# Optimization experiments

Measured on AMD Instinct MI355X. Metric: run time of the kernel, lower is better.

The kernel has to match this reference:

```python
import jax, jax.numpy as jnp
import numpy as np

D_MODEL = 1024
N_HEADS = 16
D_K = D_MODEL // N_HEADS
B, S = 2, 2048


def setup_inputs() -> dict:
    key = jax.random.key(0)
    ks = jax.random.split(key, 11)
    def lin(kw, kb, fan_in):
        bound = 1.0 / np.sqrt(fan_in)
        W = jax.random.uniform(kw, (fan_in, D_MODEL), jnp.float32, -bound, bound)
        b = jax.random.uniform(kb, (D_MODEL,), jnp.float32, -bound, bound)
        return W, b
    Wq, bq = lin(ks[0], ks[1], D_MODEL)
    Wk, bk = lin(ks[2], ks[3], D_MODEL)
    Wv, bv = lin(ks[4], ks[5], D_MODEL)
    Wo, bo = lin(ks[6], ks[7], D_MODEL)
    q = jax.random.normal(ks[8], (B, S, D_MODEL), jnp.float32)
    k = jax.random.normal(ks[9], (B, S, D_MODEL), jnp.float32)
    v = jax.random.normal(ks[10], (B, S, D_MODEL), jnp.float32)
    return {"q": q, "k": k, "v": v,
            "Wq": Wq, "bq": bq, "Wk": Wk, "bk": bk,
            "Wv": Wv, "bv": bv, "Wo": Wo, "bo": bo}


def reference(q, k, v, Wq, bq, Wk, bk, Wv, bv, Wo, bo):
    Bz, Sq, _ = q.shape
    def split_heads(x):  # [B,S,D] -> [B,H,S,d_k]
        return x.reshape(x.shape[0], x.shape[1], N_HEADS, D_K).transpose(0, 2, 1, 3)
    qh = split_heads(q @ Wq + bq)
    kh = split_heads(k @ Wk + bk)
    vh = split_heads(v @ Wv + bv)
    scores = jnp.einsum("bhqd,bhkd->bhqk", qh, kh) / jnp.sqrt(jnp.float32(D_K))
    attn = jax.nn.softmax(scores, axis=-1)
    out = jnp.einsum("bhqk,bhkd->bhqd", attn, vh)
    out = out.transpose(0, 2, 1, 3).reshape(Bz, Sq, D_MODEL)
    return out @ Wo + bo
```

## Files before the change

kernel.cpp:

```cpp
#include <hip/hip_runtime.h>
#include <hip/hip_bf16.h>
#include <stdint.h>

typedef __bf16 bf16;
typedef __bf16 bf16x8 __attribute__((ext_vector_type(8)));
typedef __bf16 bf16x4 __attribute__((ext_vector_type(4)));
typedef float  f32x4  __attribute__((ext_vector_type(4)));
typedef float  f32x16 __attribute__((ext_vector_type(16)));
typedef uint32_t u32;

#define MFMA16(a,b,c) __builtin_amdgcn_mfma_f32_16x16x32_bf16((a),(b),(c),0,0,0)
#define MFMA32(a,b,c) __builtin_amdgcn_mfma_f32_32x32x16_bf16((a),(b),(c),0,0,0)

#define QSCL 0.1803368801111204f

__device__ __forceinline__ u32 sx32(u32 x) {
    return (u32)__shfl_xor((int)x, 32, 64);
}
__device__ __forceinline__ float swapred_max(float v) {
    return fmaxf(v, __builtin_bit_cast(float, sx32(__builtin_bit_cast(u32, v))));
}
__device__ __forceinline__ float swapred_sum(float v) {
    return v + __builtin_bit_cast(float, sx32(__builtin_bit_cast(u32, v)));
}
__device__ __forceinline__ u32 pkbf(float lo, float hi) {
    union { bf16 h[2]; u32 u; } un;
    un.h[0] = (bf16)lo; un.h[1] = (bf16)hi;
    return un.u;
}
__device__ __forceinline__ void pack_frags(const float* p, int hi, bf16x8& f0, bf16x8& f1) {
    u32 k01 = pkbf(p[0],  p[1]),  k23 = pkbf(p[2],  p[3]);
    u32 k45 = pkbf(p[4],  p[5]),  k67 = pkbf(p[6],  p[7]);
    u32 k89 = pkbf(p[8],  p[9]),  kab = pkbf(p[10], p[11]);
    u32 kcd = pkbf(p[12], p[13]), kef = pkbf(p[14], p[15]);
    u32 x01 = sx32(k01), x23 = sx32(k23), x45 = sx32(k45), x67 = sx32(k67);
    u32 x89 = sx32(k89), xab = sx32(kab), xcd = sx32(kcd), xef = sx32(kef);
    union { u32 w[4]; bf16x8 v; } u0, u1;
    u0.w[0] = hi ? x45 : k01;  u0.w[1] = hi ? x67 : k23;
    u0.w[2] = hi ? k45 : x01;  u0.w[3] = hi ? k67 : x23;
    u1.w[0] = hi ? xcd : k89;  u1.w[1] = hi ? xef : kab;
    u1.w[2] = hi ? kcd : x89;  u1.w[3] = hi ? kef : xab;
    f0 = u0.v; f1 = u1.v;
}

__global__ __launch_bounds__(256) void k_cvt3(const float* __restrict__ a, const float* __restrict__ b,
                                              const float* __restrict__ c,
                                              bf16* __restrict__ x, bf16* __restrict__ y,
                                              bf16* __restrict__ z) {
    int i = blockIdx.x * 256 + threadIdx.x;
    int t = i >> 20;
    int r = (i & 1048575) << 2;
    const float* s = (t == 0) ? a : ((t == 1) ? b : c);
    bf16* d = (t == 0) ? x : ((t == 1) ? y : z);
    float4 v = *(const float4*)&s[r];
    bf16x4 w = {(bf16)v.x, (bf16)v.y, (bf16)v.z, (bf16)v.w};
    *(bf16x4*)&d[r] = w;
}
__global__ __launch_bounds__(256) void k_cvt1(const float* __restrict__ s, bf16* __restrict__ d) {
    int r = (blockIdx.x * 256 + threadIdx.x) << 2;
    float4 v = *(const float4*)&s[r];
    bf16x4 w = {(bf16)v.x, (bf16)v.y, (bf16)v.z, (bf16)v.w};
    *(bf16x4*)&d[r] = w;
}

__global__ __launch_bounds__(256) void k_transpose_w(const float* __restrict__ W,
                                                     bf16* __restrict__ Wt, float scale) {
    __shared__ bf16 t[64][65];
    const int n0 = blockIdx.x * 64, k0 = blockIdx.y * 64;
    for (int i = 0; i < 16; ++i) {
        int idx = threadIdx.x + i * 256, r = idx >> 6, c = idx & 63;
        t[r][c] = (bf16)(W[(size_t)(k0 + r) * 1024 + n0 + c] * scale);
    }
    __syncthreads();
    for (int i = 0; i < 16; ++i) {
        int idx = threadIdx.x + i * 256, r = idx >> 6, c = idx & 63;
        Wt[(size_t)(n0 + r) * 1024 + k0 + c] = t[c][r];
    }
}

__global__ __launch_bounds__(256) void k_transpose_v(const bf16* __restrict__ V,
                                                     bf16* __restrict__ Vt) {
    __shared__ bf16 t[64][65];
    const int s0 = blockIdx.x * 64, bh = blockIdx.y;
    for (int i = 0; i < 16; ++i) {
        int idx = threadIdx.x + i * 256, r = idx >> 6, c = idx & 63;
        t[r][c] = V[((size_t)bh * 2048 + s0 + r) * 64 + c];
    }
    __syncthreads();
    for (int i = 0; i < 16; ++i) {
        int idx = threadIdx.x + i * 256, r = idx >> 6, c = idx & 63;
        Vt[((size_t)bh * 64 + r) * 2048 + s0 + c] = t[c][r];
    }
}

__device__ __forceinline__ void gemm_tile(const bf16* __restrict__ A, const bf16* __restrict__ Bt,
                                          const float* __restrict__ bias, float bscale,
                                          void* __restrict__ Cp, int out_mode, int m0, int n0,
                                          bf16 (*As)[64], bf16 (*Bs)[64]) {
    const int tid = threadIdx.x;
    const int wid = tid >> 6, lane = tid & 63, lg = lane >> 4, lm = lane & 15;
    const int wr = wid >> 1, wc = wid & 1;
    const int grow = tid >> 3, gcol = (tid & 7) << 3;

    f32x4 acc[4][4] = {};

    for (int kt = 0; kt < 16; ++kt) {
        const int k0 = kt << 6;
        __syncthreads();
#pragma unroll
        for (int p = 0; p < 4; ++p) {
            __builtin_amdgcn_global_load_lds(
                (const __attribute__((address_space(1))) void*)(A + (size_t)(m0 + p * 32 + grow) * 1024 + k0 + gcol),
                (__attribute__((address_space(3))) void*)(&As[p * 32 + wid * 8][0]), 16, 0, 0);
            __builtin_amdgcn_global_load_lds(
                (const __attribute__((address_space(1))) void*)(Bt + (size_t)(n0 + p * 32 + grow) * 1024 + k0 + gcol),
                (__attribute__((address_space(3))) void*)(&Bs[p * 32 + wid * 8][0]), 16, 0, 0);
        }
        __syncthreads();
#pragma unroll
        for (int kk = 0; kk < 2; ++kk) {
            bf16x8 a[4], b[4];
#pragma unroll
            for (int i = 0; i < 4; ++i) a[i] = *(const bf16x8*)&As[wr * 64 + i * 16 + lm][kk * 32 + lg * 8];
#pragma unroll
            for (int j = 0; j < 4; ++j) b[j] = *(const bf16x8*)&Bs[wc * 64 + j * 16 + lm][kk * 32 + lg * 8];
#pragma unroll
            for (int i = 0; i < 4; ++i)
#pragma unroll
                for (int j = 0; j < 4; ++j) acc[i][j] = MFMA16(a[i], b[j], acc[i][j]);
        }
    }

    for (int i = 0; i < 4; ++i) {
        for (int j = 0; j < 4; ++j) {
            int col = n0 + wc * 64 + j * 16 + lm;
            float bv = bscale * bias[col];
            for (int q = 0; q < 4; ++q) {
                int row = m0 + wr * 64 + i * 16 + lg * 4 + q;
                float val = acc[i][j][q] + bv;
                if (out_mode == 0) {
                    int bb = row >> 11, s = row & 2047, h = col >> 6, d = col & 63;
                    ((bf16*)Cp)[(((size_t)bb * 16 + h) * 2048 + s) * 64 + d] = (bf16)val;
                } else {
                    ((float*)Cp)[(size_t)row * 1024 + col] = (float)val;
                }
            }
        }
    }
}

__device__ __forceinline__ void tile_decode(int r, int& m0, int& n0) {
    int xcd = r & 7, slot = (r >> 3) & 3, n = (r >> 5) & 7;
    m0 = (xcd * 4 + slot) * 128;
    n0 = n * 128;
}

__global__ __launch_bounds__(256, 4) void k_gemm_one(const bf16* __restrict__ A,
                                                     const bf16* __restrict__ Bt,
                                                     const float* __restrict__ bias, float bscale,
                                                     void* __restrict__ Cp, int out_mode) {
    __shared__ bf16 As[128][64];
    __shared__ bf16 Bs[128][64];
    int m0, n0;
    tile_decode(blockIdx.x, m0, n0);
    gemm_tile(A, Bt, bias, bscale, Cp, out_mode, m0, n0, As, Bs);
}

__global__ __launch_bounds__(256, 4) void k_gemm_qkv(const bf16* __restrict__ qc, const bf16* __restrict__ kc,
                                                     const bf16* __restrict__ vc,
                                                     const bf16* __restrict__ Wtq, const bf16* __restrict__ Wtk,
                                                     const bf16* __restrict__ Wtv,
                                                     const float* __restrict__ bq, const float* __restrict__ bk,
                                                     const float* __restrict__ bv,
                                                     bf16* __restrict__ Qb, bf16* __restrict__ Kb,
                                                     bf16* __restrict__ Vb) {
    __shared__ bf16 As[128][64];
    __shared__ bf16 Bs[128][64];
    int l = blockIdx.x, z = l >> 8, r = l & 255;
    int m0, n0;
    tile_decode(r, m0, n0);
    const bf16* A  = (z == 0) ? qc : ((z == 1) ? kc : vc);
    const bf16* Bt = (z == 0) ? Wtq : ((z == 1) ? Wtk : Wtv);
    const float* bias = (z == 0) ? bq : ((z == 1) ? bk : bv);
    float bscale = (z == 0) ? QSCL : 1.0f;
    bf16* Cp = (z == 0) ? Qb : ((z == 1) ? Kb : Vb);
    gemm_tile(A, Bt, bias, bscale, (void*)Cp, 0, m0, n0, As, Bs);
}

__global__ __launch_bounds__(512, 2) void k_attn(const bf16* __restrict__ Q,
                                                 const bf16* __restrict__ Kb,
                                                 const bf16* __restrict__ Vt,
                                                 bf16* __restrict__ Out) {
    __shared__ bf16 Ks[2][64 * 64];
    __shared__ bf16 Vs[2][64 * 64];
    const int tid = threadIdx.x;
    const int wid = tid >> 6, lane = tid & 63;
    const int lm = lane & 31, hi = lane >> 5;
    const int bid = blockIdx.x;
    const int bh = bid & 31, qt = bid >> 5;
    const int bb = bh >> 4, h = bh & 15;
    const int qrow = qt * 256 + wid * 32 + lm;
    const size_t qk_base = (size_t)bh * (2048 * 64);
    const size_t vt_base = (size_t)bh * (64 * 2048);

    const int srow = tid >> 3, sc8 = tid & 7;
    const int cse = (sc8 ^ (srow & 7)) * 8;
    const bf16* kstage = Kb + qk_base + (size_t)srow * 64 + cse;
    const bf16* vstage = Vt + vt_base + (size_t)srow * 2048 + cse;
    const int ldsoff = wid * 1024;

    bf16x8 qf[4];
    {
        const bf16* qp = Q + qk_base + (size_t)qrow * 64 + hi * 8;
#pragma unroll
        for (int f = 0; f < 4; ++f) qf[f] = *(const bf16x8*)(qp + f * 16);
    }

    f32x16 O0 = {}, O1 = {};
    float mrow = -1e30f, lrow = 0.f;

    const int swz = (lm & 7);

    __builtin_amdgcn_global_load_lds(
        (const __attribute__((address_space(1))) void*)(kstage),
        (__attribute__((address_space(3))) void*)((char*)&Ks[0][0] + ldsoff), 16, 0, 0);
    __builtin_amdgcn_global_load_lds(
        (const __attribute__((address_space(1))) void*)(vstage),
        (__attribute__((address_space(3))) void*)((char*)&Vs[0][0] + ldsoff), 16, 0, 0);
    __syncthreads();

    int cur = 0;
#pragma unroll 1
    for (int kt = 0; kt < 32; ++kt) {
        if (kt + 1 < 32) {
            __builtin_amdgcn_global_load_lds(
                (const __attribute__((address_space(1))) void*)(kstage + (size_t)(kt + 1) * 4096),
                (__attribute__((address_space(3))) void*)((char*)&Ks[cur ^ 1][0] + ldsoff), 16, 0, 0);
            __builtin_amdgcn_global_load_lds(
                (const __attribute__((address_space(1))) void*)(vstage + (size_t)(kt + 1) * 64),
                (__attribute__((address_space(3))) void*)((char*)&Vs[cur ^ 1][0] + ldsoff), 16, 0, 0);
        }

        const char* Ksc = (const char*)&Ks[cur][0];
        const char* Vsc = (const char*)&Vs[cur][0];

        bf16x8 kf0[4], kf1[4];
#pragma unroll
        for (int f = 0; f < 4; ++f) {
            int ch = (f << 1) | hi;
            kf0[f] = *(const bf16x8*)(Ksc + lm * 128 + ((ch ^ swz) << 4));
            kf1[f] = *(const bf16x8*)(Ksc + (lm + 32) * 128 + ((ch ^ swz) << 4));
        }
        bf16x8 vf0[4], vf1[4];
#pragma unroll
        for (int ks = 0; ks < 4; ++ks) {
            int ch = (ks << 1) | hi;
            vf0[ks] = *(const bf16x8*)(Vsc + lm * 128 + ((ch ^ swz) << 4));
            vf1[ks] = *(const bf16x8*)(Vsc + (lm + 32) * 128 + ((ch ^ swz) << 4));
        }

        f32x16 s0 = {}, s1 = {};
#pragma unroll
        for (int f = 0; f < 4; ++f) {
            s0 = MFMA32(kf0[f], qf[f], s0);
            s1 = MFMA32(kf1[f], qf[f], s1);
        }

        float t8[8];
#pragma unroll
        for (int r = 0; r < 8; ++r)
            t8[r] = fmaxf(fmaxf(s0[r], s0[r + 8]), fmaxf(s1[r], s1[r + 8]));
#pragma unroll
        for (int st = 4; st; st >>= 1)
#pragma unroll
            for (int r = 0; r < st; ++r) t8[r] = fmaxf(t8[r], t8[r + st]);
        float pm = swapred_max(t8[0]);

        if (!__all(pm <= mrow + 8.0f)) {
            float mnew = fmaxf(mrow, pm);
            float corr = __builtin_amdgcn_exp2f(mrow - mnew);
            lrow *= corr;
            O0 *= corr;
            O1 *= corr;
            mrow = mnew;
        }

        float p0a[16], p1a[16];
#pragma unroll
        for (int r = 0; r < 16; ++r) p0a[r] = __builtin_amdgcn_exp2f(s0[r] - mrow);
#pragma unroll
        for (int r = 0; r < 16; ++r) p1a[r] = __builtin_amdgcn_exp2f(s1[r] - mrow);
        float u8[8];
#pragma unroll
        for (int r = 0; r < 8; ++r) u8[r] = (p0a[r] + p0a[r + 8]) + (p1a[r] + p1a[r + 8]);
#pragma unroll
        for (int st = 4; st; st >>= 1)
#pragma unroll
            for (int r = 0; r < st; ++r) u8[r] = u8[r] + u8[r + st];
        lrow += swapred_sum(u8[0]);

        bf16x8 pf[4];
        pack_frags(p0a, hi, pf[0], pf[1]);
        pack_frags(p1a, hi, pf[2], pf[3]);

#pragma unroll
        for (int ks = 0; ks < 4; ++ks) {
            O0 = MFMA32(vf0[ks], pf[ks], O0);
            O1 = MFMA32(vf1[ks], pf[ks], O1);
        }

        __syncthreads();
        cur ^= 1;
    }

    float inv = 1.0f / lrow;
    bf16* op = Out + ((size_t)bb * 2048 + qrow) * 1024 + h * 64 + 4 * hi;
#pragma unroll
    for (int t = 0; t < 4; ++t) {
        bf16x4 w0, w1;
#pragma unroll
        for (int e = 0; e < 4; ++e) {
            w0[e] = (bf16)(O0[4 * t + e] * inv);
            w1[e] = (bf16)(O1[4 * t + e] * inv);
        }
        *(bf16x4*)(op + 8 * t)      = w0;
        *(bf16x4*)(op + 32 + 8 * t) = w1;
    }
}

extern "C" void kernel_launch(void* const* d_in, const int* in_sizes, int n_in,
                              void* d_out, int out_size, void* d_ws, size_t ws_size,
                              hipStream_t stream) {
    const float* q  = (const float*)d_in[0];
    const float* k  = (const float*)d_in[1];
    const float* v  = (const float*)d_in[2];
    const float* Wq = (const float*)d_in[3];
    const float* bq = (const float*)d_in[4];
    const float* Wk = (const float*)d_in[5];
    const float* bk = (const float*)d_in[6];
    const float* Wv = (const float*)d_in[7];
    const float* bv = (const float*)d_in[8];
    const float* Wo = (const float*)d_in[9];
    const float* bo = (const float*)d_in[10];

    char* ws = (char*)d_ws;
    const size_t MB = 1ull << 20;
    const dim3 twg(16, 16), blk(256);

    if (ws_size >= 64 * MB) {
        bf16* Wtq = (bf16*)(ws + 0 * MB);
        bf16* Wtk = (bf16*)(ws + 2 * MB);
        bf16* Wtv = (bf16*)(ws + 4 * MB);
        bf16* Wto = (bf16*)(ws + 6 * MB);
        bf16* qc  = (bf16*)(ws + 8 * MB);
        bf16* kc  = (bf16*)(ws + 16 * MB);
        bf16* vc  = (bf16*)(ws + 24 * MB);
        bf16* Qb  = (bf16*)(ws + 32 * MB);
        bf16* Kb  = (bf16*)(ws + 40 * MB);
        bf16* Vb  = (bf16*)(ws + 48 * MB);
        bf16* Vtb = (bf16*)(ws + 56 * MB);
        bf16* AOb = kc;

        k_transpose_w<<<twg, blk, 0, stream>>>(Wq, Wtq, QSCL);
        k_transpose_w<<<twg, blk, 0, stream>>>(Wk, Wtk, 1.0f);
        k_transpose_w<<<twg, blk, 0, stream>>>(Wv, Wtv, 1.0f);
        k_transpose_w<<<twg, blk, 0, stream>>>(Wo, Wto, 1.0f);
        k_cvt3<<<12288, blk, 0, stream>>>(q, k, v, qc, kc, vc);
        k_gemm_qkv<<<768, blk, 0, stream>>>(qc, kc, vc, Wtq, Wtk, Wtv, bq, bk, bv, Qb, Kb, Vb);
        k_transpose_v<<<dim3(32, 32), blk, 0, stream>>>(Vb, Vtb);
        k_attn<<<256, 512, 0, stream>>>(Qb, Kb, Vtb, AOb);
        k_gemm_one<<<256, blk, 0, stream>>>(AOb, Wto, bo, 1.0f, d_out, 1);
    } else {
        bf16* Wt   = (bf16*)(ws + 0 * MB);
        bf16* Qb   = (bf16*)(ws + 2 * MB);
        bf16* Kb   = (bf16*)(ws + 10 * MB);
        bf16* Vtb  = (bf16*)(ws + 18 * MB);
        bf16* AOb  = (bf16*)(ws + 26 * MB);
        bf16* Cb   = Vtb;
        bf16* Vb   = (bf16*)d_out;

        k_cvt1<<<4096, blk, 0, stream>>>(q, Cb);
        k_transpose_w<<<twg, blk, 0, stream>>>(Wq, Wt, QSCL);
        k_gemm_one<<<256, blk, 0, stream>>>(Cb, Wt, bq, QSCL, (void*)Qb, 0);
        k_cvt1<<<4096, blk, 0, stream>>>(k, Cb);
        k_transpose_w<<<twg, blk, 0, stream>>>(Wk, Wt, 1.0f);
        k_gemm_one<<<256, blk, 0, stream>>>(Cb, Wt, bk, 1.0f, (void*)Kb, 0);
        k_cvt1<<<4096, blk, 0, stream>>>(v, Cb);
        k_transpose_w<<<twg, blk, 0, stream>>>(Wv, Wt, 1.0f);
        k_gemm_one<<<256, blk, 0, stream>>>(Cb, Wt, bv, 1.0f, (void*)Vb, 0);
        k_transpose_v<<<dim3(32, 32), blk, 0, stream>>>(Vb, Vtb);
        k_transpose_w<<<twg, blk, 0, stream>>>(Wo, Wt, 1.0f);
        k_attn<<<256, 512, 0, stream>>>(Qb, Kb, Vtb, AOb);
        k_gemm_one<<<256, blk, 0, stream>>>(AOb, Wt, bo, 1.0f, d_out, 1);
    }
}
```

Baseline: 152.9 us.

## Fuse V transpose into QKV GEMM, retile output GEMM, speculate softmax exp

The V projection is now computed as Wv^T·v^T, so the GEMM epilogue writes V already transposed into the per-head layout and the separate transpose kernel and its buffer are gone. The output projection gets its own kernel with 128x64 tiles and 512 blocks, giving more blocks for the CUs. In attention, the exponentials are computed before the max check and only recomputed when the running max changes, and the cross-half row-sum shuffle is deferred to the end. The transposed V epilogue writes scattered 2-byte stores, which may be uncoalesced.

```diff
diff --git a/kernel.cpp b/kernel.cpp
--- a/kernel.cpp
+++ b/kernel.cpp
@@ -78,21 +78,6 @@
     }
 }
 
-__global__ __launch_bounds__(256) void k_transpose_v(const bf16* __restrict__ V,
-                                                     bf16* __restrict__ Vt) {
-    __shared__ bf16 t[64][65];
-    const int s0 = blockIdx.x * 64, bh = blockIdx.y;
-    for (int i = 0; i < 16; ++i) {
-        int idx = threadIdx.x + i * 256, r = idx >> 6, c = idx & 63;
-        t[r][c] = V[((size_t)bh * 2048 + s0 + r) * 64 + c];
-    }
-    __syncthreads();
-    for (int i = 0; i < 16; ++i) {
-        int idx = threadIdx.x + i * 256, r = idx >> 6, c = idx & 63;
-        Vt[((size_t)bh * 64 + r) * 2048 + s0 + c] = t[c][r];
-    }
-}
-
 __device__ __forceinline__ void gemm_tile(const bf16* __restrict__ A, const bf16* __restrict__ Bt,
                                           const float* __restrict__ bias, float bscale,
                                           void* __restrict__ Cp, int out_mode, int m0, int n0,
@@ -134,15 +119,16 @@
     for (int i = 0; i < 4; ++i) {
         for (int j = 0; j < 4; ++j) {
             int col = n0 + wc * 64 + j * 16 + lm;
-            float bv = bscale * bias[col];
             for (int q = 0; q < 4; ++q) {
                 int row = m0 + wr * 64 + i * 16 + lg * 4 + q;
-                float val = acc[i][j][q] + bv;
                 if (out_mode == 0) {
+                    float val = acc[i][j][q] + bscale * bias[col];
                     int bb = row >> 11, s = row & 2047, h = col >> 6, d = col & 63;
                     ((bf16*)Cp)[(((size_t)bb * 16 + h) * 2048 + s) * 64 + d] = (bf16)val;
                 } else {
-                    ((float*)Cp)[(size_t)row * 1024 + col] = (float)val;
+                    float val = acc[i][j][q] + bias[row];
+                    size_t idx = (((size_t)(col >> 11) * 16 + (row >> 6)) * 64 + (row & 63)) * 2048 + (col & 2047);
+                    ((bf16*)Cp)[idx] = (bf16)val;
                 }
             }
         }
@@ -154,16 +140,33 @@
     m0 = (xcd * 4 + slot) * 128;
     n0 = n * 128;
 }
-
-__global__ __launch_bounds__(256, 4) void k_gemm_one(const bf16* __restrict__ A,
-                                                     const bf16* __restrict__ Bt,
-                                                     const float* __restrict__ bias, float bscale,
-                                                     void* __restrict__ Cp, int out_mode) {
+__device__ __forceinline__ void tile_decode_vt(int r, int& m0, int& n0) {
+    int xcd = r & 7, loc = r >> 3;
+    int nslot = loc & 3, m = loc >> 2;
+    n0 = (xcd * 4 + nslot) * 128;
+    m0 = m * 128;
+}
+
+__global__ __launch_bounds__(256, 4) void k_gemm_proj(const bf16* __restrict__ A,
+                                                      const bf16* __restrict__ Bt,
+                                                      const float* __restrict__ bias, float bscale,
+                                                      void* __restrict__ Cp) {
     __shared__ bf16 As[128][64];
     __shared__ bf16 Bs[128][64];
     int m0, n0;
     tile_decode(blockIdx.x, m0, n0);
-    gemm_tile(A, Bt, bias, bscale, Cp, out_mode, m0, n0, As, Bs);
+    gemm_tile(A, Bt, bias, bscale, Cp, 0, m0, n0, As, Bs);
+}
+
+__global__ __launch_bounds__(256, 4) void k_gemm_vt(const bf16* __restrict__ Wtv,
+                                                    const bf16* __restrict__ vc,
+                                                    const float* __restrict__ bias,
+                                                    bf16* __restrict__ Vtb) {
+    __shared__ bf16 As[128][64];
+    __shared__ bf16 Bs[128][64];
+    int m0, n0;
+    tile_decode_vt(blockIdx.x, m0, n0);
+    gemm_tile(Wtv, vc, bias, 1.0f, (void*)Vtb, 2, m0, n0, As, Bs);
 }
 
 __global__ __launch_bounds__(256, 4) void k_gemm_qkv(const bf16* __restrict__ qc, const bf16* __restrict__ kc,
@@ -173,18 +176,79 @@
                                                      const float* __restrict__ bq, const float* __restrict__ bk,
                                                      const float* __restrict__ bv,
                                                      bf16* __restrict__ Qb, bf16* __restrict__ Kb,
-                                                     bf16* __restrict__ Vb) {
+                                                     bf16* __restrict__ Vtb) {
     __shared__ bf16 As[128][64];
     __shared__ bf16 Bs[128][64];
     int l = blockIdx.x, z = l >> 8, r = l & 255;
     int m0, n0;
-    tile_decode(r, m0, n0);
-    const bf16* A  = (z == 0) ? qc : ((z == 1) ? kc : vc);
-    const bf16* Bt = (z == 0) ? Wtq : ((z == 1) ? Wtk : Wtv);
-    const float* bias = (z == 0) ? bq : ((z == 1) ? bk : bv);
-    float bscale = (z == 0) ? QSCL : 1.0f;
-    bf16* Cp = (z == 0) ? Qb : ((z == 1) ? Kb : Vb);
-    gemm_tile(A, Bt, bias, bscale, (void*)Cp, 0, m0, n0, As, Bs);
+    if (z == 2) {
+        tile_decode_vt(r, m0, n0);
+        gemm_tile(Wtv, vc, bv, 1.0f, (void*)Vtb, 2, m0, n0, As, Bs);
+    } else {
+        tile_decode(r, m0, n0);
+        const bf16* A  = (z == 0) ? qc : kc;
+        const bf16* Bt = (z == 0) ? Wtq : Wtk;
+        const float* bias = (z == 0) ? bq : bk;
+        float bscale = (z == 0) ? QSCL : 1.0f;
+        bf16* Cp = (z == 0) ? Qb : Kb;
+        gemm_tile(A, Bt, bias, bscale, (void*)Cp, 0, m0, n0, As, Bs);
+    }
+}
+
+__global__ __launch_bounds__(256, 4) void k_gemm_out(const bf16* __restrict__ A,
+                                                     const bf16* __restrict__ Bt,
+                                                     const float* __restrict__ bias,
+                                                     float* __restrict__ C) {
+    __shared__ bf16 As[128][64];
+    __shared__ bf16 Bs[64][64];
+    const int tid = threadIdx.x;
+    const int wid = tid >> 6, lane = tid & 63, lg = lane >> 4, lm = lane & 15;
+    const int grow = tid >> 3, gcol = (tid & 7) << 3;
+    const int r = blockIdx.x;
+    const int xcd = r & 7, loc = r >> 3;
+    const int mslot = loc & 3, n = loc >> 2;
+    const int m0 = (xcd * 4 + mslot) * 128, n0 = n * 64;
+
+    f32x4 acc[2][4] = {};
+
+    for (int kt = 0; kt < 16; ++kt) {
+        const int k0 = kt << 6;
+        __syncthreads();
+#pragma unroll
+        for (int p = 0; p < 4; ++p)
+            __builtin_amdgcn_global_load_lds(
+                (const __attribute__((address_space(1))) void*)(A + (size_t)(m0 + p * 32 + grow) * 1024 + k0 + gcol),
+                (__attribute__((address_space(3))) void*)(&As[p * 32 + wid * 8][0]), 16, 0, 0);
+#pragma unroll
+        for (int p = 0; p < 2; ++p)
+            __builtin_amdgcn_global_load_lds(
+                (const __attribute__((address_space(1))) void*)(Bt + (size_t)(n0 + p * 32 + grow) * 1024 + k0 + gcol),
+                (__attribute__((address_space(3))) void*)(&Bs[p * 32 + wid * 8][0]), 16, 0, 0);
+        __syncthreads();
+#pragma unroll
+        for (int kk = 0; kk < 2; ++kk) {
+            bf16x8 a[2], b[4];
+#pragma unroll
+            for (int i = 0; i < 2; ++i) a[i] = *(const bf16x8*)&As[wid * 32 + i * 16 + lm][kk * 32 + lg * 8];
+#pragma unroll
+            for (int j = 0; j < 4; ++j) b[j] = *(const bf16x8*)&Bs[j * 16 + lm][kk * 32 + lg * 8];
+#pragma unroll
+            for (int i = 0; i < 2; ++i)
+#pragma unroll
+                for (int j = 0; j < 4; ++j) acc[i][j] = MFMA16(a[i], b[j], acc[i][j]);
+        }
+    }
+
+    for (int i = 0; i < 2; ++i) {
+        for (int j = 0; j < 4; ++j) {
+            int col = n0 + j * 16 + lm;
+            float bv = bias[col];
+            for (int q = 0; q < 4; ++q) {
+                int row = m0 + wid * 32 + i * 16 + lg * 4 + q;
+                C[(size_t)row * 1024 + col] = acc[i][j][q] + bv;
+            }
+        }
+    }
 }
 
 __global__ __launch_bounds__(512, 2) void k_attn(const bf16* __restrict__ Q,
@@ -217,7 +281,7 @@
     }
 
     f32x16 O0 = {}, O1 = {};
-    float mrow = -1e30f, lrow = 0.f;
+    float mrow = -1e30f, lsum = 0.f;
 
     const int swz = (lm & 7);
 
@@ -266,6 +330,12 @@
             s1 = MFMA32(kf1[f], qf[f], s1);
         }
 
+        float pe0[16], pe1[16];
+#pragma unroll
+        for (int r = 0; r < 16; ++r) pe0[r] = __builtin_amdgcn_exp2f(s0[r] - mrow);
+#pragma unroll
+        for (int r = 0; r < 16; ++r) pe1[r] = __builtin_amdgcn_exp2f(s1[r] - mrow);
+
         float t8[8];
 #pragma unroll
         for (int r = 0; r < 8; ++r)
@@ -279,29 +349,28 @@
         if (!__all(pm <= mrow + 8.0f)) {
             float mnew = fmaxf(mrow, pm);
             float corr = __builtin_amdgcn_exp2f(mrow - mnew);
-            lrow *= corr;
+            lsum *= corr;
             O0 *= corr;
             O1 *= corr;
             mrow = mnew;
-        }
-
-        float p0a[16], p1a[16];
-#pragma unroll
-        for (int r = 0; r < 16; ++r) p0a[r] = __builtin_amdgcn_exp2f(s0[r] - mrow);
-#pragma unroll
-        for (int r = 0; r < 16; ++r) p1a[r] = __builtin_amdgcn_exp2f(s1[r] - mrow);
+#pragma unroll
+            for (int r = 0; r < 16; ++r) pe0[r] = __builtin_amdgcn_exp2f(s0[r] - mrow);
+#pragma unroll
+            for (int r = 0; r < 16; ++r) pe1[r] = __builtin_amdgcn_exp2f(s1[r] - mrow);
+        }
+
         float u8[8];
 #pragma unroll
-        for (int r = 0; r < 8; ++r) u8[r] = (p0a[r] + p0a[r + 8]) + (p1a[r] + p1a[r + 8]);
+        for (int r = 0; r < 8; ++r) u8[r] = (pe0[r] + pe0[r + 8]) + (pe1[r] + pe1[r + 8]);
 #pragma unroll
         for (int st = 4; st; st >>= 1)
 #pragma unroll
             for (int r = 0; r < st; ++r) u8[r] = u8[r] + u8[r + st];
-        lrow += swapred_sum(u8[0]);
+        lsum += u8[0];
 
         bf16x8 pf[4];
-        pack_frags(p0a, hi, pf[0], pf[1]);
-        pack_frags(p1a, hi, pf[2], pf[3]);
+        pack_frags(pe0, hi, pf[0], pf[1]);
+        pack_frags(pe1, hi, pf[2], pf[3]);
 
 #pragma unroll
         for (int ks = 0; ks < 4; ++ks) {
@@ -313,6 +382,7 @@
         cur ^= 1;
     }
 
+    float lrow = swapred_sum(lsum);
     float inv = 1.0f / lrow;
     bf16* op = Out + ((size_t)bb * 2048 + qrow) * 1024 + h * 64 + 4 * hi;
 #pragma unroll
@@ -357,8 +427,7 @@
         bf16* vc  = (bf16*)(ws + 24 * MB);
         bf16* Qb  = (bf16*)(ws + 32 * MB);
         bf16* Kb  = (bf16*)(ws + 40 * MB);
-        bf16* Vb  = (bf16*)(ws + 48 * MB);
-        bf16* Vtb = (bf16*)(ws + 56 * MB);
+        bf16* Vtb = (bf16*)(ws + 48 * MB);
         bf16* AOb = kc;
 
         k_transpose_w<<<twg, blk, 0, stream>>>(Wq, Wtq, QSCL);
@@ -366,31 +435,28 @@
         k_transpose_w<<<twg, blk, 0, stream>>>(Wv, Wtv, 1.0f);
         k_transpose_w<<<twg, blk, 0, stream>>>(Wo, Wto, 1.0f);
         k_cvt3<<<12288, blk, 0, stream>>>(q, k, v, qc, kc, vc);
-        k_gemm_qkv<<<768, blk, 0, stream>>>(qc, kc, vc, Wtq, Wtk, Wtv, bq, bk, bv, Qb, Kb, Vb);
-        k_transpose_v<<<dim3(32, 32), blk, 0, stream>>>(Vb, Vtb);
+        k_gemm_qkv<<<768, blk, 0, stream>>>(qc, kc, vc, Wtq, Wtk, Wtv, bq, bk, bv, Qb, Kb, Vtb);
         k_attn<<<256, 512, 0, stream>>>(Qb, Kb, Vtb, AOb);
-        k_gemm_one<<<256, blk, 0, stream>>>(AOb, Wto, bo, 1.0f, d_out, 1);
+        k_gemm_out<<<512, blk, 0, stream>>>(AOb, Wto, bo, (float*)d_out);
     } else {
         bf16* Wt   = (bf16*)(ws + 0 * MB);
         bf16* Qb   = (bf16*)(ws + 2 * MB);
         bf16* Kb   = (bf16*)(ws + 10 * MB);
         bf16* Vtb  = (bf16*)(ws + 18 * MB);
         bf16* AOb  = (bf16*)(ws + 26 * MB);
-        bf16* Cb   = Vtb;
-        bf16* Vb   = (bf16*)d_out;
+        bf16* Cb   = (bf16*)d_out;
 
         k_cvt1<<<4096, blk, 0, stream>>>(q, Cb);
         k_transpose_w<<<twg, blk, 0, stream>>>(Wq, Wt, QSCL);
-        k_gemm_one<<<256, blk, 0, stream>>>(Cb, Wt, bq, QSCL, (void*)Qb, 0);
+        k_gemm_proj<<<256, blk, 0, stream>>>(Cb, Wt, bq, QSCL, (void*)Qb);
         k_cvt1<<<4096, blk, 0, stream>>>(k, Cb);
         k_transpose_w<<<twg, blk, 0, stream>>>(Wk, Wt, 1.0f);
-        k_gemm_one<<<256, blk, 0, stream>>>(Cb, Wt, bk, 1.0f, (void*)Kb, 0);
+        k_gemm_proj<<<256, blk, 0, stream>>>(Cb, Wt, bk, 1.0f, (void*)Kb);
         k_cvt1<<<4096, blk, 0, stream>>>(v, Cb);
         k_transpose_w<<<twg, blk, 0, stream>>>(Wv, Wt, 1.0f);
-        k_gemm_one<<<256, blk, 0, stream>>>(Cb, Wt, bv, 1.0f, (void*)Vb, 0);
-        k_transpose_v<<<dim3(32, 32), blk, 0, stream>>>(Vb, Vtb);
+        k_gemm_vt<<<256, blk, 0, stream>>>(Wt, Cb, bv, Vtb);
         k_transpose_w<<<twg, blk, 0, stream>>>(Wo, Wt, 1.0f);
         k_attn<<<256, 512, 0, stream>>>(Qb, Kb, Vtb, AOb);
-        k_gemm_one<<<256, blk, 0, stream>>>(AOb, Wt, bo, 1.0f, d_out, 1);
-    }
-}
+        k_gemm_out<<<512, blk, 0, stream>>>(AOb, Wt, bo, (float*)d_out);
+    }
+}
```

Measured after the change: 144.2 us. -5.7%, faster.
